# Performance work log

Measured on AMD Instinct MI355X. Metric: run time of the kernel, lower is better.

## Reference

```python
import jax, jax.numpy as jnp
import numpy as np

B, T, I, H = 64, 512, 256, 1024


def setup_inputs() -> dict:
    key = jax.random.key(0)
    ks = jax.random.split(key, 20)
    stdv = float(1.0 / np.sqrt(H))
    u = lambda k, shape: jax.random.uniform(k, shape, jnp.float32, -stdv, stdv)
    d = {
        "inputs": jax.random.normal(ks[0], (B, T, I), jnp.float32),
        "h0": jax.random.normal(ks[1], (1, B, H), jnp.float32),
        "c0": jax.random.normal(ks[2], (1, B, H), jnp.float32),
    }
    names = ["w_ii", "w_hi", "b_ii", "b_hi",
             "w_if", "w_hf", "b_if", "b_hf",
             "w_io", "w_ho", "b_io", "b_ho",
             "w_ig", "w_hg", "b_ig", "b_hg"]
    shapes = {"w_i": (H, I), "w_h": (H, H), "b_i": (H,), "b_h": (H,)}
    for j, n in enumerate(names):
        d[n] = u(ks[3 + j], shapes[n[:3]])
    return d


def reference(inputs, h0, c0,
              w_ii, w_hi, b_ii, b_hi,
              w_if, w_hf, b_if, b_hf,
              w_io, w_ho, b_io, b_ho,
              w_ig, w_hg, b_ig, b_hg):
    # Fuse the 4 gate GEMMs into one: gate order i, f, g, o.
    Wx = jnp.concatenate([w_ii, w_if, w_ig, w_io], axis=0)  # (4H, I)
    Wh = jnp.concatenate([w_hi, w_hf, w_hg, w_ho], axis=0)  # (4H, H)
    b = jnp.concatenate([b_ii + b_hi, b_if + b_hf, b_ig + b_hg, b_io + b_ho], axis=0)  # (4H,)
    # Precompute all input projections in one big GEMM: (T, B, 4H)
    x_proj = jnp.einsum('bti,gi->tbg', inputs, Wx) + b

    def step(carry, xp):
        h, c = carry                       # (B, H), (B, H)
        z = xp + h @ Wh.T                  # (B, 4H)
        i = jax.nn.sigmoid(z[:, :H])
        f = jax.nn.sigmoid(z[:, H:2 * H])
        g = jnp.tanh(z[:, 2 * H:3 * H])
        o = jax.nn.sigmoid(z[:, 3 * H:])
        c = f * c + i * g
        h = o * jnp.tanh(c)
        return (h, c), h

    (h, c), hs = jax.lax.scan(step, (h0[0], c0[0]), x_proj)
    hidden_seq = jnp.transpose(hs, (1, 0, 2))  # (B, T, H)
    return hidden_seq, (h[None], c[None])
```

## Files before the change

### kernel.cpp

```cpp
#include <hip/hip_runtime.h>
#include <hip/hip_bf16.h>

#define TT 512
#define BB 64
#define II 256
#define HH 1024
#define NWG 256
#define MB 16
#define NJ 16
#define NR 64
#define KTOT 1280
#define HROWB 2048
#define NFLAG 1024
#define MAXTRY (1 << 20)

typedef __bf16 bf16x8 __attribute__((ext_vector_type(8)));
typedef float f32x4 __attribute__((ext_vector_type(4)));
typedef unsigned uint32x4 __attribute__((ext_vector_type(4)));
typedef unsigned uint32x2 __attribute__((ext_vector_type(2)));

__device__ inline uint32x4 ld16_sc1(const void* p) {
  uint32x4 r;
  asm volatile("global_load_dwordx4 %0, %1, off sc1" : "=&v"(r) : "v"(p));
  return r;
}


__global__ __launch_bounds__(256) void k_cast_inputs(const float* __restrict__ in,
                                                     __hip_bfloat16* __restrict__ outp) {
  int i = (blockIdx.x * 256 + threadIdx.x) * 4;
  float4 v = *reinterpret_cast<const float4*>(in + i);
  outp[i + 0] = __float2bfloat16(v.x);
  outp[i + 1] = __float2bfloat16(v.y);
  outp[i + 2] = __float2bfloat16(v.z);
  outp[i + 3] = __float2bfloat16(v.w);
}

__global__ __launch_bounds__(256) void k_pack_w(
    const float* __restrict__ wxi, const float* __restrict__ whi,
    const float* __restrict__ wxf, const float* __restrict__ whf,
    const float* __restrict__ wxg, const float* __restrict__ whg,
    const float* __restrict__ wxo, const float* __restrict__ who,
    __hip_bfloat16* __restrict__ Wp) {
  int t = blockIdx.x * 256 + threadIdx.x;
  int p = t / 320;
  int k4 = (t - p * 320) * 4;
  int j = p >> 2, gate = p & 3;
  const float* wx = (gate == 0) ? wxi : (gate == 1) ? wxf : (gate == 2) ? wxg : wxo;
  const float* wh = (gate == 0) ? whi : (gate == 1) ? whf : (gate == 2) ? whg : who;
  float4 v;
  if (k4 < II) v = *reinterpret_cast<const float4*>(wx + (size_t)j * II + k4);
  else         v = *reinterpret_cast<const float4*>(wh + (size_t)j * HH + (k4 - II));
  __hip_bfloat16* o = Wp + (size_t)p * KTOT + k4;
  o[0] = __float2bfloat16(v.x);
  o[1] = __float2bfloat16(v.y);
  o[2] = __float2bfloat16(v.z);
  o[3] = __float2bfloat16(v.w);
}

__global__ __launch_bounds__(256) void k_pack_bias_h0(
    const float* __restrict__ bii, const float* __restrict__ bhi,
    const float* __restrict__ bif, const float* __restrict__ bhf,
    const float* __restrict__ bg,  const float* __restrict__ bhg,
    const float* __restrict__ bio, const float* __restrict__ bho,
    const float* __restrict__ h0, float* __restrict__ biasp,
    __hip_bfloat16* __restrict__ hb, unsigned* __restrict__ flags) {
  int i = blockIdx.x * 256 + threadIdx.x;
  if (i < 4096) {
    int j = i >> 2, gate = i & 3;
    const float* bi = (gate == 0) ? bii : (gate == 1) ? bif : (gate == 2) ? bg : bio;
    const float* bh = (gate == 0) ? bhi : (gate == 1) ? bhf : (gate == 2) ? bhg : bho;
    biasp[i] = bi[j] + bh[j];
  }
  if (i < NFLAG) flags[i] = 0;
  hb[i] = __float2bfloat16(h0[i]);
}


__global__ __launch_bounds__(256, 1) void k_lstm(
    const __hip_bfloat16* __restrict__ xb,
    const __hip_bfloat16* __restrict__ Wp,
    const float* __restrict__ biasp,
    const float* __restrict__ c0,
    __hip_bfloat16* __restrict__ hbuf,
    unsigned* __restrict__ flags,
    float* __restrict__ out)
{
  extern __shared__ __align__(16) char smem[];
  char* Hs = smem;
  char* Zx = smem + 32768;
  char* Ho = smem + 37888;

  const int tid = threadIdx.x;
  const int lane = tid & 63;
  const int wq = tid >> 6;
  const int bt = blockIdx.x >> 6;
  const int gt = blockIdx.x & 63;
  const int b0 = bt * MB;
  const int r0 = gt * NR;

  const int l15 = lane & 15;
  const int kqu = lane >> 4;

  const int brow = r0 + wq * 16 + l15;
  bf16x8 wxr[8], whr[32];
  {
    const __hip_bfloat16* ws = Wp + (size_t)brow * KTOT + kqu * 8;
#pragma unroll
    for (int kk = 0; kk < 8; ++kk)
      wxr[kk] = *reinterpret_cast<const bf16x8*>(ws + kk * 32);
    const __hip_bfloat16* wh = ws + II;
#pragma unroll
    for (int kk = 0; kk < 32; ++kk)
      whr[kk] = *reinterpret_cast<const bf16x8*>(wh + kk * 32);
  }

  const int m_e = 4 * kqu + (lane & 3);
  const int tq = (lane >> 2) & 3;
  const int j_g = gt * NJ + wq * 4 + tq;
  const int b_g = b0 + m_e;
  const float4 bias = *reinterpret_cast<const float4*>(biasp + j_g * 4);
  float c_reg = c0[(size_t)b_g * HH + j_g];

  const int hs_swz = l15 & 7;
  char* ZxW = Zx + wq * 1280;
  char* HoW = Ho + wq * 128;

  {
    uint32x4 tmp[8];
#pragma unroll
    for (int q = 0; q < 8; ++q) {
      int idx = q * 64 + lane;
      int rl = wq * 4 + (idx >> 7);
      int u = idx & 127;
      tmp[q] = ld16_sc1(hbuf + (size_t)(b0 + rl) * HH + u * 8);
    }
    asm volatile("s_waitcnt vmcnt(0)" ::: "memory");
    __builtin_amdgcn_sched_barrier(0);
#pragma unroll
    for (int q = 0; q < 8; ++q) {
      int idx = q * 64 + lane;
      int rl = wq * 4 + (idx >> 7);
      int u = idx & 127;
      *reinterpret_cast<uint32x4*>(Hs + rl * HROWB + ((u ^ (rl & 7)) << 4)) = tmp[q];
    }
  }

  const __hip_bfloat16* xrowA = xb + (size_t)(b0 + l15) * (TT * II) + kqu * 8;
  f32x4 accs[4];
#pragma unroll
  for (int q = 0; q < 4; ++q) accs[q] = (f32x4){0.f, 0.f, 0.f, 0.f};
#pragma unroll
  for (int kk = 0; kk < 8; ++kk) {
    bf16x8 xa = *reinterpret_cast<const bf16x8*>(xrowA + kk * 32);
    accs[kk & 3] = __builtin_amdgcn_mfma_f32_16x16x32_bf16(xa, wxr[kk], accs[kk & 3], 0, 0, 0);
  }

  __syncthreads();

  for (int t = 0; t < TT; ++t) {
#pragma unroll
    for (int kk = 0; kk < 32; ++kk) {
      int u = kk * 4 + kqu;
      bf16x8 a = *reinterpret_cast<const bf16x8*>(Hs + l15 * HROWB + ((u ^ hs_swz) << 4));
      accs[kk & 3] = __builtin_amdgcn_mfma_f32_16x16x32_bf16(a, whr[kk], accs[kk & 3], 0, 0, 0);
    }
    f32x4 acc = (accs[0] + accs[1]) + (accs[2] + accs[3]);

    *reinterpret_cast<f32x4*>(ZxW + l15 * 80 + kqu * 16) = acc;
    asm volatile("s_waitcnt lgkmcnt(0)" ::: "memory");
    __builtin_amdgcn_sched_barrier(0);
    float zi = *reinterpret_cast<const float*>(ZxW + (4 * tq + 0) * 80 + m_e * 4) + bias.x;
    float zf = *reinterpret_cast<const float*>(ZxW + (4 * tq + 1) * 80 + m_e * 4) + bias.y;
    float zg = *reinterpret_cast<const float*>(ZxW + (4 * tq + 2) * 80 + m_e * 4) + bias.z;
    float zo = *reinterpret_cast<const float*>(ZxW + (4 * tq + 3) * 80 + m_e * 4) + bias.w;

    float ig = 1.f / (1.f + __expf(-zi));
    float fg = 1.f / (1.f + __expf(-zf));
    float gg = 2.f / (1.f + __expf(-2.f * zg)) - 1.f;
    float og = 1.f / (1.f + __expf(-zo));
    c_reg = fg * c_reg + ig * gg;
    float tc = 2.f / (1.f + __expf(-2.f * c_reg)) - 1.f;
    float h = og * tc;

    if (t == TT - 1) {
      out[(size_t)b_g * (TT * HH) + (size_t)t * HH + j_g] = h;
      out[(size_t)BB * TT * HH + (size_t)b_g * HH + j_g] = h;
      out[(size_t)BB * TT * HH + BB * HH + (size_t)b_g * HH + j_g] = c_reg;
      break;
    }

    __hip_bfloat16 hb16 = __float2bfloat16(h);
    *reinterpret_cast<unsigned short*>(HoW + m_e * 8 + tq * 2) =
        *reinterpret_cast<unsigned short*>(&hb16);
    asm volatile("s_waitcnt lgkmcnt(0)" ::: "memory");
    __builtin_amdgcn_sched_barrier(0);

    const int nxt = (t + 1) & 1;
    const unsigned gen = (unsigned)(t + 1);
    if (lane < 16) {
      uint32x2 hv = *reinterpret_cast<const uint32x2*>(HoW + lane * 8);
      __hip_bfloat16* dst = hbuf + (size_t)nxt * (BB * HH)
                          + (size_t)(b0 + lane) * HH + gt * NJ + wq * 4;
      asm volatile("global_store_dwordx2 %0, %1, off sc1" :: "v"(dst), "v"(hv) : "memory");
    }
    asm volatile("s_waitcnt vmcnt(0)" ::: "memory");
    if (lane == 0) {
      asm volatile("global_store_dword %0, %1, off sc1"
                   :: "v"(flags + bt * 256 + gt * 4 + wq), "v"(gen) : "memory");
    }

    out[(size_t)b_g * (TT * HH) + (size_t)t * HH + j_g] = h;
#pragma unroll
    for (int q = 0; q < 4; ++q) accs[q] = (f32x4){0.f, 0.f, 0.f, 0.f};
    {
      const __hip_bfloat16* xp = xrowA + (size_t)(t + 1) * II;
#pragma unroll
      for (int kk = 0; kk < 8; ++kk) {
        bf16x8 xa = *reinterpret_cast<const bf16x8*>(xp + kk * 32);
        accs[kk & 3] = __builtin_amdgcn_mfma_f32_16x16x32_bf16(xa, wxr[kk], accs[kk & 3], 0, 0, 0);
      }
    }

    {
      const unsigned* fp = flags + bt * 256 + lane * 4;
      int tries = 0;
      uint32x4 f;
      for (;;) {
        asm volatile("global_load_dwordx4 %0, %1, off sc1\n\ts_waitcnt vmcnt(0)"
                     : "=&v"(f) : "v"(fp) : "memory");
        int ok = (f.x >= gen) && (f.y >= gen) && (f.z >= gen) && (f.w >= gen);
        if (__all(ok) || ++tries > MAXTRY) break;
      }
    }

    {
      uint32x4 tmp[8];
      const __hip_bfloat16* hsrc = hbuf + (size_t)nxt * (BB * HH);
#pragma unroll
      for (int q = 0; q < 8; ++q) {
        int idx = q * 64 + lane;
        int rl = wq * 4 + (idx >> 7);
        int u = idx & 127;
        tmp[q] = ld16_sc1(hsrc + (size_t)(b0 + rl) * HH + u * 8);
      }
      asm volatile("s_waitcnt vmcnt(0)" ::: "memory");
      __builtin_amdgcn_sched_barrier(0);
#pragma unroll
      for (int q = 0; q < 8; ++q) {
        int idx = q * 64 + lane;
        int rl = wq * 4 + (idx >> 7);
        int u = idx & 127;
        *reinterpret_cast<uint32x4*>(Hs + rl * HROWB + ((u ^ (rl & 7)) << 4)) = tmp[q];
      }
    }
    __syncthreads();
  }
}


extern "C" void kernel_launch(void* const* d_in, const int* in_sizes, int n_in,
                              void* d_out, int out_size, void* d_ws, size_t ws_size,
                              hipStream_t stream) {
  (void)in_sizes; (void)n_in; (void)out_size; (void)ws_size;
  const float* inputs = (const float*)d_in[0];
  const float* h0 = (const float*)d_in[1];
  const float* c0 = (const float*)d_in[2];
  const float* w_ii = (const float*)d_in[3];
  const float* w_hi = (const float*)d_in[4];
  const float* b_ii = (const float*)d_in[5];
  const float* b_hi = (const float*)d_in[6];
  const float* w_if = (const float*)d_in[7];
  const float* w_hf = (const float*)d_in[8];
  const float* b_if = (const float*)d_in[9];
  const float* b_hf = (const float*)d_in[10];
  const float* w_io = (const float*)d_in[11];
  const float* w_ho = (const float*)d_in[12];
  const float* b_io = (const float*)d_in[13];
  const float* b_ho = (const float*)d_in[14];
  const float* w_ig = (const float*)d_in[15];
  const float* w_hg = (const float*)d_in[16];
  const float* b_ig = (const float*)d_in[17];
  const float* b_hg = (const float*)d_in[18];

  char* ws = (char*)d_ws;
  __hip_bfloat16* xb    = (__hip_bfloat16*)ws;
  __hip_bfloat16* Wp    = (__hip_bfloat16*)(ws + 16777216);
  float*          biasp = (float*)(ws + 27262976);
  __hip_bfloat16* hbuf  = (__hip_bfloat16*)(ws + 27279360);
  unsigned*       flags = (unsigned*)(ws + 27541504);
  float* out = (float*)d_out;

  k_cast_inputs<<<8192, 256, 0, stream>>>(inputs, xb);
  k_pack_w<<<5120, 256, 0, stream>>>(w_ii, w_hi, w_if, w_hf, w_ig, w_hg, w_io, w_ho, Wp);
  k_pack_bias_h0<<<256, 256, 0, stream>>>(b_ii, b_hi, b_if, b_hf, b_ig, b_hg,
                                          b_io, b_ho, h0, biasp, hbuf, flags);

  const int lds_bytes = 131072;
  hipFuncSetAttribute((const void*)k_lstm,
                      hipFuncAttributeMaxDynamicSharedMemorySize, lds_bytes);
  void* args[] = {(void*)&xb, (void*)&Wp, (void*)&biasp, (void*)&c0,
                  (void*)&hbuf, (void*)&flags, (void*)&out};
  hipError_t e = hipLaunchCooperativeKernel((void*)k_lstm, dim3(NWG), dim3(256),
                                            args, lds_bytes, stream);
  if (e != hipSuccess) {
    k_lstm<<<dim3(NWG), dim3(256), lds_bytes, stream>>>(xb, Wp, biasp, c0, hbuf, flags, out);
  }
}
```

Measured before the change: 1.904 ms.

## Split hidden-state reload into halves and overlap with recurrent MFMA

Each step's reload of the exchanged hidden state now happens in two halves. The first half of the K dimension is loaded into LDS and its MFMAs start while the second half's global loads are still in flight. The x-projection loads for the next step are issued before the flag store and the spin-wait, so their latency hides behind synchronization. The flag store now waits only on the h store rather than on all outstanding loads. In exchange, the schedule depends on hand-placed vmcnt counts and an extra barrier per step.

Result: slower. 4.364 ms (+129.2%).

```diff
diff --git a/kernel.cpp b/kernel.cpp
--- a/kernel.cpp
+++ b/kernel.cpp
@@ -22,6 +22,11 @@
 __device__ inline uint32x4 ld16_sc1(const void* p) {
   uint32x4 r;
   asm volatile("global_load_dwordx4 %0, %1, off sc1" : "=&v"(r) : "v"(p));
+  return r;
+}
+__device__ inline uint32x4 ld16(const void* p) {
+  uint32x4 r;
+  asm volatile("global_load_dwordx4 %0, %1, off" : "=&v"(r) : "v"(p) : "memory");
   return r;
 }
 
@@ -130,18 +135,16 @@
     uint32x4 tmp[8];
 #pragma unroll
     for (int q = 0; q < 8; ++q) {
-      int idx = q * 64 + lane;
-      int rl = wq * 4 + (idx >> 7);
-      int u = idx & 127;
+      int rl = wq * 4 + (q & 3);
+      int u = (q >> 2) * 64 + lane;
       tmp[q] = ld16_sc1(hbuf + (size_t)(b0 + rl) * HH + u * 8);
     }
     asm volatile("s_waitcnt vmcnt(0)" ::: "memory");
     __builtin_amdgcn_sched_barrier(0);
 #pragma unroll
     for (int q = 0; q < 8; ++q) {
-      int idx = q * 64 + lane;
-      int rl = wq * 4 + (idx >> 7);
-      int u = idx & 127;
+      int rl = wq * 4 + (q & 3);
+      int u = (q >> 2) * 64 + lane;
       *reinterpret_cast<uint32x4*>(Hs + rl * HROWB + ((u ^ (rl & 7)) << 4)) = tmp[q];
     }
   }
@@ -158,9 +161,16 @@
 
   __syncthreads();
 
+#pragma unroll
+  for (int kk = 0; kk < 16; ++kk) {
+    int u = kk * 4 + kqu;
+    bf16x8 a = *reinterpret_cast<const bf16x8*>(Hs + l15 * HROWB + ((u ^ hs_swz) << 4));
+    accs[kk & 3] = __builtin_amdgcn_mfma_f32_16x16x32_bf16(a, whr[kk], accs[kk & 3], 0, 0, 0);
+  }
+
   for (int t = 0; t < TT; ++t) {
 #pragma unroll
-    for (int kk = 0; kk < 32; ++kk) {
+    for (int kk = 16; kk < 32; ++kk) {
       int u = kk * 4 + kqu;
       bf16x8 a = *reinterpret_cast<const bf16x8*>(Hs + l15 * HROWB + ((u ^ hs_swz) << 4));
       accs[kk & 3] = __builtin_amdgcn_mfma_f32_16x16x32_bf16(a, whr[kk], accs[kk & 3], 0, 0, 0);
@@ -204,22 +214,19 @@
                           + (size_t)(b0 + lane) * HH + gt * NJ + wq * 4;
       asm volatile("global_store_dwordx2 %0, %1, off sc1" :: "v"(dst), "v"(hv) : "memory");
     }
-    asm volatile("s_waitcnt vmcnt(0)" ::: "memory");
+
+    out[(size_t)b_g * (TT * HH) + (size_t)t * HH + j_g] = h;
+    uint32x4 tmpx[8];
+    {
+      const __hip_bfloat16* xp = xrowA + (size_t)(t + 1) * II;
+#pragma unroll
+      for (int kk = 0; kk < 8; ++kk)
+        tmpx[kk] = ld16(xp + kk * 32);
+    }
+    asm volatile("s_waitcnt vmcnt(8)" ::: "memory");
     if (lane == 0) {
       asm volatile("global_store_dword %0, %1, off sc1"
                    :: "v"(flags + bt * 256 + gt * 4 + wq), "v"(gen) : "memory");
-    }
-
-    out[(size_t)b_g * (TT * HH) + (size_t)t * HH + j_g] = h;
-#pragma unroll
-    for (int q = 0; q < 4; ++q) accs[q] = (f32x4){0.f, 0.f, 0.f, 0.f};
-    {
-      const __hip_bfloat16* xp = xrowA + (size_t)(t + 1) * II;
-#pragma unroll
-      for (int kk = 0; kk < 8; ++kk) {
-        bf16x8 xa = *reinterpret_cast<const bf16x8*>(xp + kk * 32);
-        accs[kk & 3] = __builtin_amdgcn_mfma_f32_16x16x32_bf16(xa, wxr[kk], accs[kk & 3], 0, 0, 0);
-      }
     }
 
     {
@@ -233,28 +240,53 @@
         if (__all(ok) || ++tries > MAXTRY) break;
       }
     }
-
+    __builtin_amdgcn_sched_barrier(0);
+
+    uint32x4 tmp[8];
     {
-      uint32x4 tmp[8];
       const __hip_bfloat16* hsrc = hbuf + (size_t)nxt * (BB * HH);
 #pragma unroll
       for (int q = 0; q < 8; ++q) {
-        int idx = q * 64 + lane;
-        int rl = wq * 4 + (idx >> 7);
-        int u = idx & 127;
+        int rl = wq * 4 + (q & 3);
+        int u = (q >> 2) * 64 + lane;
         tmp[q] = ld16_sc1(hsrc + (size_t)(b0 + rl) * HH + u * 8);
       }
-      asm volatile("s_waitcnt vmcnt(0)" ::: "memory");
-      __builtin_amdgcn_sched_barrier(0);
-#pragma unroll
-      for (int q = 0; q < 8; ++q) {
-        int idx = q * 64 + lane;
-        int rl = wq * 4 + (idx >> 7);
-        int u = idx & 127;
-        *reinterpret_cast<uint32x4*>(Hs + rl * HROWB + ((u ^ (rl & 7)) << 4)) = tmp[q];
-      }
-    }
-    __syncthreads();
+    }
+#pragma unroll
+    for (int q = 0; q < 4; ++q) accs[q] = (f32x4){0.f, 0.f, 0.f, 0.f};
+#pragma unroll
+    for (int kk = 0; kk < 8; ++kk) {
+      bf16x8 xa = __builtin_bit_cast(bf16x8, tmpx[kk]);
+      accs[kk & 3] = __builtin_amdgcn_mfma_f32_16x16x32_bf16(xa, wxr[kk], accs[kk & 3], 0, 0, 0);
+    }
+    __builtin_amdgcn_sched_barrier(0);
+
+    asm volatile("s_waitcnt vmcnt(4)" ::: "memory");
+    __builtin_amdgcn_sched_barrier(0);
+#pragma unroll
+    for (int q = 0; q < 4; ++q) {
+      int rl = wq * 4 + q;
+      *reinterpret_cast<uint32x4*>(Hs + rl * HROWB + ((lane ^ (rl & 7)) << 4)) = tmp[q];
+    }
+    asm volatile("s_waitcnt lgkmcnt(0)" ::: "memory");
+    __builtin_amdgcn_s_barrier();
+
+#pragma unroll
+    for (int kk = 0; kk < 16; ++kk) {
+      int u = kk * 4 + kqu;
+      bf16x8 a = *reinterpret_cast<const bf16x8*>(Hs + l15 * HROWB + ((u ^ hs_swz) << 4));
+      accs[kk & 3] = __builtin_amdgcn_mfma_f32_16x16x32_bf16(a, whr[kk], accs[kk & 3], 0, 0, 0);
+    }
+
+    asm volatile("s_waitcnt vmcnt(0)" ::: "memory");
+    __builtin_amdgcn_sched_barrier(0);
+#pragma unroll
+    for (int q = 4; q < 8; ++q) {
+      int rl = wq * 4 + (q & 3);
+      *reinterpret_cast<uint32x4*>(Hs + rl * HROWB + (((64 + lane) ^ (rl & 7)) << 4)) = tmp[q];
+    }
+    asm volatile("s_waitcnt lgkmcnt(0)" ::: "memory");
+    __builtin_amdgcn_s_barrier();
   }
 }
 
```
